# Kernel optimization log

Measured on AMD Instinct MI355X. Metric: run time of the kernel, lower is better.

The kernel has to match this reference:

```python
import jax, jax.numpy as jnp
import numpy as np

B, C, H, W = 2, 256, 128, 128
L, NH, NP = 4, 8, 4
D = C // NH
HW = H * W


def _pos_emb_2d(h, w, c):
    # positional_encodings.PositionalEncoding2D for channels-last input (B, h, w, c)
    ch = int(np.ceil(c / 4) * 2)
    inv_freq = 1.0 / (10000.0 ** (np.arange(0, ch, 2, dtype=np.float32) / ch))

    def emb(n):
        s = np.arange(n, dtype=np.float32)[:, None] * inv_freq[None, :]
        return np.stack([np.sin(s), np.cos(s)], -1).reshape(n, -1)  # interleaved sin/cos

    out = np.zeros((h, w, 2 * ch), np.float32)
    out[:, :, :ch] = emb(h)[:, None, :]
    out[:, :, ch:2 * ch] = emb(w)[None, :, :]
    return jnp.asarray(out[:, :, :c])


def _offset_bias():
    # init_weights grid_init bias of sampling_offsets
    thetas = np.arange(NH, dtype=np.float32) * (2.0 * np.pi / NH)
    g = np.stack([np.cos(thetas), np.sin(thetas)], -1)
    g = g / np.abs(g).max(-1, keepdims=True)
    g = np.tile(g[:, None, None, :], (1, 1, NP, 1))
    for i in range(NP):
        g[:, :, i, :] *= i + 1
    return np.tile(g.reshape(-1)[None], (L, 1)).astype(np.float32)


def _ref_points(h, w):
    # get_reference_points with scale_ratio == 1 (ratio of equal lidar ranges)
    ry, rx = jnp.meshgrid(jnp.linspace(0.5, h - 0.5, h) / h,
                          jnp.linspace(0.5, w - 0.5, w) / w, indexing='ij')
    return jnp.stack([rx.reshape(-1), ry.reshape(-1)], -1)  # (HW, 2) as (x, y)


def _deform_attn(value, loc, aw, h, w):
    # value: (B,HW,NH,D); loc in [0,1]: (B,HW,NH,NP,2); aw: (B,HW,NH,NP)
    # Matches F.grid_sample(mode='bilinear', padding_mode='zeros', align_corners=False)
    b, q, nh, d = value.shape
    p = loc.shape[3]
    v = value.transpose(0, 2, 1, 3)  # (B, NH, HW, D)
    gx = 2.0 * loc[..., 0] - 1.0
    gy = 2.0 * loc[..., 1] - 1.0
    ix = ((gx + 1.0) * w - 1.0) * 0.5
    iy = ((gy + 1.0) * h - 1.0) * 0.5
    x0 = jnp.floor(ix)
    y0 = jnp.floor(iy)

    def gather(xf, yf):
        valid = (xf >= 0) & (xf <= w - 1) & (yf >= 0) & (yf <= h - 1)
        xi = jnp.clip(xf, 0, w - 1).astype(jnp.int32)
        yi = jnp.clip(yf, 0, h - 1).astype(jnp.int32)
        idx = (yi * w + xi).transpose(0, 2, 1, 3).reshape(b, nh, q * p)
        g = jnp.take_along_axis(v, idx[..., None], axis=2).reshape(b, nh, q, p, d)
        return g * valid.transpose(0, 2, 1, 3)[..., None]

    wx1 = (ix - x0).transpose(0, 2, 1, 3)[..., None]
    wy1 = (iy - y0).transpose(0, 2, 1, 3)[..., None]
    wx0 = 1.0 - wx1
    wy0 = 1.0 - wy1
    s = (gather(x0, y0) * (wx0 * wy0) + gather(x0 + 1.0, y0) * (wx1 * wy0)
         + gather(x0, y0 + 1.0) * (wx0 * wy1) + gather(x0 + 1.0, y0 + 1.0) * (wx1 * wy1))
    out = jnp.einsum('bhqpd,bqhp->bqhd', s, aw)
    return out.reshape(b, q, nh * d)


def setup_inputs() -> dict:
    key = jax.random.key(0)
    ks = jax.random.split(key, 8)
    sc = 1.0 / np.sqrt(C).astype(np.float32)
    return {
        "ego_feature": jax.random.normal(ks[0], (B, C, H, W), jnp.float32),
        "conv_w": jax.random.normal(ks[1], (C, C), jnp.float32) * sc,  # 1x1 conv, (in,out)
        "conv_b": jnp.zeros((C,), jnp.float32),
        "in_scale": jnp.ones((1,), jnp.float32) / 30.0,
        "out_scale": jnp.ones((1,), jnp.float32) / 30.0,
        "off_w": jax.random.normal(ks[2], (L, C, NH * NP * 2), jnp.float32) * 0.01,
        "off_b": jnp.asarray(_offset_bias()),
        "aw_w": jax.random.normal(ks[3], (L, C, NH * NP), jnp.float32) * 0.02,
        "aw_b": jnp.zeros((L, NH * NP), jnp.float32),
        "vp_w": jax.random.normal(ks[4], (L, C, C), jnp.float32) * sc,
        "vp_b": jnp.zeros((L, C), jnp.float32),
        "op_w": jax.random.normal(ks[5], (L, C, C), jnp.float32) * sc,
        "op_b": jnp.zeros((L, C), jnp.float32),
    }


def reference(ego_feature, conv_w, conv_b, in_scale, out_scale, off_w, off_b,
              aw_w, aw_b, vp_w, vp_b, op_w, op_b):
    # PositionalEncodingPermute2D: channels-last PE, permuted to (C,H,W)
    pe_in = _pos_emb_2d(H, W, C).transpose(2, 0, 1)[None]  # (1,C,H,W)
    x = ego_feature + in_scale[0] * pe_in
    key_tok = x.reshape(B, C, HW).transpose(0, 2, 1)  # (B, HW, C)
    # Upsample(scale=1) is identity; 1x1 conv == per-token matmul
    out = key_tok @ conv_w + conv_b
    pe_out = _pos_emb_2d(H, W, C)[None]  # (1,H,W,C)
    ref = _ref_points(H, W)
    norm = jnp.asarray([W, H], jnp.float32)
    for l in range(L):
        o = out.reshape(B, H, W, C) + out_scale[0] * pe_out
        q = o.reshape(B, HW, C)
        identity = q
        v = (key_tok @ vp_w[l] + vp_b[l]).reshape(B, HW, NH, D)
        offs = (q @ off_w[l] + off_b[l]).reshape(B, HW, NH, NP, 2)
        aw = jax.nn.softmax((q @ aw_w[l] + aw_b[l]).reshape(B, HW, NH, NP), axis=-1)
        loc = ref[None, :, None, None, :] + offs / norm
        attn = _deform_attn(v, loc, aw, H, W)
        out = attn @ op_w[l] + op_b[l] + identity  # dropout is identity in eval
    return out  # (B, HW, C)
```

## Files before the change

kernel.cpp:

```cpp
#include <hip/hip_runtime.h>
#include <math.h>

#define HH 128
#define WW 128
#define CCH 256
#define NHH 8
#define NPP 4
#define DDIM 32
#define HWW (HH * WW)
#define BB 2
#define MM (BB * HWW)
#define KK 256

typedef __attribute__((ext_vector_type(8))) __bf16 bf16x8;
typedef __attribute__((ext_vector_type(8))) short s16x8;
typedef __attribute__((ext_vector_type(4))) short s16x4;
typedef __attribute__((ext_vector_type(4))) float f32x4;

#define PE_LOG2_STEP 0.20762050593f

__device__ __forceinline__ float pe_val(int c, int y, int x) {
    int j = (c & 127) >> 1;
    float pos = (c < 128) ? (float)y : (float)x;
    float f = exp2f(-(float)j * PE_LOG2_STEP);
    float s, cs;
    __sincosf(pos * f, &s, &cs);
    return (c & 1) ? cs : s;
}

__device__ __forceinline__ short f2b(float f) {
    union { float f; unsigned u; } c; c.f = f;
    unsigned r = c.u + 0x7FFF + ((c.u >> 16) & 1);
    return (short)(r >> 16);
}

__device__ __forceinline__ float b2f(short s) {
    union { unsigned u; float f; } c;
    c.u = ((unsigned)(unsigned short)s) << 16;
    return c.f;
}

__device__ __forceinline__ void gload16(const short* g, short* l) {
    __builtin_amdgcn_global_load_lds(
        (const __attribute__((address_space(1))) unsigned int*)g,
        (__attribute__((address_space(3))) unsigned int*)l, 16, 0, 0);
}

__global__ __launch_bounds__(256) void pe_table_kernel(
    const float* __restrict__ out_scale, short* __restrict__ pe_b)
{
    int t = blockIdx.x * 256 + threadIdx.x;
    int cp = t & 127;
    int p = t >> 7;
    int y = p >> 7, x = p & 127;
    int c2 = cp * 2;
    int j = (c2 & 127) >> 1;
    float pos = (c2 < 128) ? (float)y : (float)x;
    float f = exp2f(-(float)j * PE_LOG2_STEP);
    float s, c;
    __sincosf(pos * f, &s, &c);
    float sc = out_scale[0];
    pe_b[(size_t)p * CCH + c2] = f2b(sc * s);
    pe_b[(size_t)p * CCH + c2 + 1] = f2b(sc * c);
}

__global__ __launch_bounds__(256) void convert_big_w(
    const float* __restrict__ conv_w, const float* __restrict__ vp_w,
    const float* __restrict__ op_w, short* __restrict__ wt)
{
    __shared__ float tile[32][33];
    int z = blockIdx.z;
    const float* src = (z == 0) ? conv_w
                     : (z <= 4) ? vp_w + (size_t)(z - 1) * KK * CCH
                                : op_w + (size_t)(z - 5) * KK * CCH;
    short* dst = wt + (size_t)z * KK * CCH;
    int k0 = blockIdx.x * 32, n0 = blockIdx.y * 32;
    int tx = threadIdx.x, ty = threadIdx.y;
    #pragma unroll
    for (int i = 0; i < 4; ++i)
        tile[ty + i * 8][tx] = src[(size_t)(k0 + ty + i * 8) * CCH + n0 + tx];
    __syncthreads();
    int t = ty * 32 + tx;
    int n_l = t >> 3, ks = (t & 7) * 4;
    s16x4 o;
    #pragma unroll
    for (int j = 0; j < 4; ++j) o[j] = f2b(tile[ks + j][n_l]);
    *(s16x4*)&dst[(size_t)(n0 + n_l) * KK + k0 + ks] = o;
}

__global__ __launch_bounds__(256) void convert_offaw_w(
    const float* __restrict__ off_w, const float* __restrict__ aw_w,
    const float* __restrict__ off_b, const float* __restrict__ aw_b,
    short* __restrict__ wt, float* __restrict__ bias_cat)
{
    __shared__ float tile[32][33];
    int l = blockIdx.z;
    int nt = blockIdx.y;
    int k0 = blockIdx.x * 32;
    const float* src; int N, ncol0;
    if (nt < 2) { src = off_w + (size_t)l * KK * 64; N = 64; ncol0 = nt * 32; }
    else        { src = aw_w + (size_t)l * KK * 32; N = 32; ncol0 = 0; }
    int tx = threadIdx.x, ty = threadIdx.y;
    #pragma unroll
    for (int i = 0; i < 4; ++i)
        tile[ty + i * 8][tx] = src[(size_t)(k0 + ty + i * 8) * N + ncol0 + tx];
    __syncthreads();
    int t = ty * 32 + tx;
    int n_l = t >> 3, ks = (t & 7) * 4;
    s16x4 o;
    #pragma unroll
    for (int j = 0; j < 4; ++j) o[j] = f2b(tile[ks + j][n_l]);
    *(s16x4*)&wt[((size_t)l * 96 + nt * 32 + n_l) * KK + k0 + ks] = o;
    if (blockIdx.x == 0 && t < 32) {
        int col = nt * 32 + t;
        bias_cat[l * 96 + col] = (nt < 2) ? off_b[l * 64 + ncol0 + t]
                                          : aw_b[l * 32 + t];
    }
}

__global__ __launch_bounds__(256) void transpose_pe_kernel(
    const float* __restrict__ ego, const float* __restrict__ in_scale,
    short* __restrict__ ktb)
{
    __shared__ float tile[32][33];
    int b = blockIdx.z;
    int c0 = blockIdx.x * 32;
    int p0 = blockIdx.y * 32;
    int tx = threadIdx.x, ty = threadIdx.y;
    const float* egob = ego + (size_t)b * CCH * HWW;
    #pragma unroll
    for (int i = 0; i < 4; ++i)
        tile[ty + i * 8][tx] = egob[(size_t)(c0 + ty + i * 8) * HWW + p0 + tx];
    __syncthreads();
    float isc = in_scale[0];
    int t = ty * 32 + tx;
    int p_l = t >> 3, cs = (t & 7) * 4;
    int p = p0 + p_l;
    int y = p >> 7, x = p & 127;
    s16x4 o;
    #pragma unroll
    for (int j = 0; j < 4; ++j) {
        int c = c0 + cs + j;
        o[j] = f2b(tile[cs + j][p_l] + isc * pe_val(c, y, x));
    }
    *(s16x4*)&ktb[((size_t)b * HWW + p) * CCH + c0 + cs] = o;
}

template<int BN, int WM, int WN>
__device__ __forceinline__ void gemm_core_reg(
    const short* __restrict__ A, const short* __restrict__ Bt,
    short* As, short* Bs, int m0, int n0, int tid,
    f32x4 (&acc)[WM / 16][WN / 16])
{
    constexpr int MF = WM / 16, NF = WN / 16;
    constexpr int WAVES_N = BN / WN;
    constexpr int BTASK = BN / 32;
    int w = tid >> 6, lane = tid & 63;
    int g = lane >> 4, l16 = lane & 15;
    int wr = w / WAVES_N, wc = w % WAVES_N;

    s16x8 ra[4];
    s16x8 rb[BTASK];
    #pragma unroll
    for (int i = 0; i < 4; ++i) {
        int task = tid + i * 256; int r = task >> 3, s = task & 7;
        ra[i] = *(const s16x8*)(A + (size_t)(m0 + r) * KK + s * 8);
    }
    #pragma unroll
    for (int i = 0; i < BTASK; ++i) {
        int task = tid + i * 256; int r = task >> 3, s = task & 7;
        rb[i] = *(const s16x8*)(Bt + (size_t)(n0 + r) * KK + s * 8);
    }

    for (int ks = 0; ks < 4; ++ks) {
        __syncthreads();
        #pragma unroll
        for (int i = 0; i < 4; ++i) {
            int task = tid + i * 256; int r = task >> 3, s = task & 7;
            *(s16x8*)&As[r * 64 + ((s ^ (r & 7)) * 8)] = ra[i];
        }
        #pragma unroll
        for (int i = 0; i < BTASK; ++i) {
            int task = tid + i * 256; int r = task >> 3, s = task & 7;
            *(s16x8*)&Bs[r * 64 + ((s ^ (r & 7)) * 8)] = rb[i];
        }
        __syncthreads();
        if (ks < 3) {
            #pragma unroll
            for (int i = 0; i < 4; ++i) {
                int task = tid + i * 256; int r = task >> 3, s = task & 7;
                ra[i] = *(const s16x8*)(A + (size_t)(m0 + r) * KK + (ks + 1) * 64 + s * 8);
            }
            #pragma unroll
            for (int i = 0; i < BTASK; ++i) {
                int task = tid + i * 256; int r = task >> 3, s = task & 7;
                rb[i] = *(const s16x8*)(Bt + (size_t)(n0 + r) * KK + (ks + 1) * 64 + s * 8);
            }
        }
        #pragma unroll
        for (int kh = 0; kh < 2; ++kh) {
            bf16x8 af[MF], bfr[NF];
            #pragma unroll
            for (int mf = 0; mf < MF; ++mf) {
                int r = wr * WM + mf * 16 + l16, s = kh * 4 + g;
                af[mf] = *(const bf16x8*)(As + r * 64 + ((s ^ (r & 7)) * 8));
            }
            #pragma unroll
            for (int nf = 0; nf < NF; ++nf) {
                int r = wc * WN + nf * 16 + l16, s = kh * 4 + g;
                bfr[nf] = *(const bf16x8*)(Bs + r * 64 + ((s ^ (r & 7)) * 8));
            }
            #pragma unroll
            for (int mf = 0; mf < MF; ++mf)
                #pragma unroll
                for (int nf = 0; nf < NF; ++nf)
                    acc[mf][nf] = __builtin_amdgcn_mfma_f32_16x16x32_bf16(
                        af[mf], bfr[nf], acc[mf][nf], 0, 0, 0);
        }
    }
}

template<int NINST>
__device__ __forceinline__ void stage_tile(
    const short* __restrict__ src, short* dst, int row0, int ks, int w, int lane)
{
    #pragma unroll
    for (int i = 0; i < NINST; ++i) {
        int c = w * 64 + i * 256;
        int cc = c + lane;
        int r = cc >> 3, u = cc & 7;
        gload16(src + (size_t)(row0 + r) * KK + ks * 64 + ((u ^ (r & 7)) << 3),
                dst + c * 8);
    }
}

template<int BM, int BN, int WM, int WN>
__device__ __forceinline__ void gemm_core_db(
    const short* __restrict__ A, const short* __restrict__ Bt,
    short* AsBase, short* BsBase, int m0, int n0, int tid,
    f32x4 (&acc)[WM / 16][WN / 16])
{
    constexpr int MF = WM / 16, NF = WN / 16;
    constexpr int WAVES_N = BN / WN;
    constexpr int A_INST = (BM * 8) / 256;
    constexpr int B_INST = (BN * 8) / 256;
    int w = tid >> 6, lane = tid & 63;
    int g = lane >> 4, l16 = lane & 15;
    int wr = w / WAVES_N, wc = w % WAVES_N;
    short* As0 = AsBase; short* As1 = AsBase + BM * 64;
    short* Bs0 = BsBase; short* Bs1 = BsBase + BN * 64;

    stage_tile<A_INST>(A, As0, m0, 0, w, lane);
    stage_tile<B_INST>(Bt, Bs0, n0, 0, w, lane);
    asm volatile("s_waitcnt vmcnt(0)" ::: "memory");
    __syncthreads();

    #pragma unroll
    for (int ks = 0; ks < 4; ++ks) {
        short* Ac = (ks & 1) ? As1 : As0;
        short* Bc = (ks & 1) ? Bs1 : Bs0;
        short* An = (ks & 1) ? As0 : As1;
        short* Bn = (ks & 1) ? Bs0 : Bs1;
        if (ks < 3) {
            stage_tile<A_INST>(A, An, m0, ks + 1, w, lane);
            stage_tile<B_INST>(Bt, Bn, n0, ks + 1, w, lane);
        }
        #pragma unroll
        for (int kh = 0; kh < 2; ++kh) {
            bf16x8 af[MF], bfr[NF];
            #pragma unroll
            for (int mf = 0; mf < MF; ++mf) {
                int r = wr * WM + mf * 16 + l16, s = kh * 4 + g;
                af[mf] = *(const bf16x8*)(Ac + r * 64 + ((s ^ (r & 7)) * 8));
            }
            #pragma unroll
            for (int nf = 0; nf < NF; ++nf) {
                int r = wc * WN + nf * 16 + l16, s = kh * 4 + g;
                bfr[nf] = *(const bf16x8*)(Bc + r * 64 + ((s ^ (r & 7)) * 8));
            }
            #pragma unroll
            for (int mf = 0; mf < MF; ++mf)
                #pragma unroll
                for (int nf = 0; nf < NF; ++nf)
                    acc[mf][nf] = __builtin_amdgcn_mfma_f32_16x16x32_bf16(
                        af[mf], bfr[nf], acc[mf][nf], 0, 0, 0);
        }
        if (ks < 3) {
            __builtin_amdgcn_sched_barrier(0);
            asm volatile("s_waitcnt vmcnt(0)" ::: "memory");
            __syncthreads();
        }
    }
}

__global__ __launch_bounds__(256) void gemm_conv_v(
    const short* __restrict__ ktb, const short* __restrict__ wt_big,
    const float* __restrict__ conv_b, const float* __restrict__ vp_b,
    const short* __restrict__ pe_b, short* __restrict__ qb,
    short* __restrict__ vb16)
{
    __shared__ short As[128 * 64];
    __shared__ short Bs[128 * 64];
    int tid = threadIdx.x;
    int flat = blockIdx.x;
    int xcd = flat & 7;
    int idx = flat >> 3;
    int mloc = idx & 31;
    int rest = idx >> 5;
    int n0 = (rest & 1) * 128;
    int z = rest >> 1;
    int m0 = (xcd * 32 + mloc) * 128;

    f32x4 acc[4][4] = {};
    gemm_core_reg<128, 64, 64>(ktb, wt_big + (size_t)z * KK * CCH, As, Bs, m0, n0, tid, acc);

    int w = tid >> 6, lane = tid & 63;
    int g = lane >> 4, l16 = lane & 15;
    int wr = w >> 1, wc = w & 1;
    const float* bias = (z == 0) ? conv_b : vp_b + (size_t)(z - 1) * CCH;
    short* vz = vb16 + (size_t)(z - 1) * MM * CCH;
    #pragma unroll
    for (int mf = 0; mf < 4; ++mf) {
        #pragma unroll
        for (int nf = 0; nf < 4; ++nf) {
            int col = n0 + wc * 64 + nf * 16 + l16;
            float bv = bias[col];
            #pragma unroll
            for (int j = 0; j < 4; ++j) {
                int row = m0 + wr * 64 + mf * 16 + g * 4 + j;
                float vv = acc[mf][nf][j] + bv;
                if (z == 0) {
                    int p = row & (HWW - 1);
                    qb[(size_t)row * CCH + col] =
                        f2b(vv + b2f(pe_b[(size_t)p * CCH + col]));
                } else {
                    int b = row >> 14, p = row & (HWW - 1);
                    int h = col >> 5, d = col & 31;
                    vz[(((size_t)(b * NHH + h)) * HWW + p) * DDIM + d] = f2b(vv);
                }
            }
        }
    }
}

__global__ __launch_bounds__(256) void gemm_scores(
    const short* __restrict__ qb, const short* __restrict__ wt,
    const float* __restrict__ bias, float* __restrict__ scores)
{
    __shared__ short As[2 * 64 * 64];
    __shared__ short Bs[2 * 96 * 64];
    int tid = threadIdx.x;
    int m0 = blockIdx.y * 64;
    f32x4 acc[2][3] = {};
    gemm_core_db<64, 96, 32, 48>(qb, wt, As, Bs, m0, 0, tid, acc);

    int w = tid >> 6, lane = tid & 63;
    int g = lane >> 4, l16 = lane & 15;
    int wr = w >> 1, wc = w & 1;
    #pragma unroll
    for (int mf = 0; mf < 2; ++mf) {
        #pragma unroll
        for (int nf = 0; nf < 3; ++nf) {
            int col = wc * 48 + nf * 16 + l16;
            float bv = bias[col];
            #pragma unroll
            for (int j = 0; j < 4; ++j) {
                int row = m0 + wr * 32 + mf * 16 + g * 4 + j;
                scores[(size_t)row * 96 + col] = acc[mf][nf][j] + bv;
            }
        }
    }
}

template<bool FINAL>
__global__ __launch_bounds__(256) void gemm_op(
    const short* __restrict__ attnb, const short* __restrict__ wt,
    const float* __restrict__ bias, const short* __restrict__ pe_b,
    float* __restrict__ outf, short* __restrict__ qb)
{
    __shared__ short As[2 * 128 * 64];
    __shared__ short Bs[2 * 128 * 64];
    int tid = threadIdx.x;
    int flat = blockIdx.x;
    int xcd = flat & 7;
    int idx = flat >> 3;
    int mloc = idx & 31;
    int n0 = (idx >> 5) * 128;
    int m0 = (xcd * 32 + mloc) * 128;
    f32x4 acc[4][4] = {};
    gemm_core_db<128, 128, 64, 64>(attnb, wt, As, Bs, m0, n0, tid, acc);

    int w = tid >> 6, lane = tid & 63;
    int g = lane >> 4, l16 = lane & 15;
    int wr = w >> 1, wc = w & 1;
    #pragma unroll
    for (int mf = 0; mf < 4; ++mf) {
        #pragma unroll
        for (int nf = 0; nf < 4; ++nf) {
            int col = n0 + wc * 64 + nf * 16 + l16;
            float bv = bias[col];
            #pragma unroll
            for (int j = 0; j < 4; ++j) {
                int row = m0 + wr * 64 + mf * 16 + g * 4 + j;
                float vv = acc[mf][nf][j] + bv + b2f(qb[(size_t)row * CCH + col]);
                if (FINAL) {
                    outf[(size_t)row * CCH + col] = vv;
                } else {
                    int p = row & (HWW - 1);
                    qb[(size_t)row * CCH + col] =
                        f2b(vv + b2f(pe_b[(size_t)p * CCH + col]));
                }
            }
        }
    }
}

__device__ __forceinline__ void fma8(uint4 u, float w, float* a) {
    a[0] = fmaf(__uint_as_float(u.x << 16), w, a[0]);
    a[1] = fmaf(__uint_as_float(u.x & 0xffff0000u), w, a[1]);
    a[2] = fmaf(__uint_as_float(u.y << 16), w, a[2]);
    a[3] = fmaf(__uint_as_float(u.y & 0xffff0000u), w, a[3]);
    a[4] = fmaf(__uint_as_float(u.z << 16), w, a[4]);
    a[5] = fmaf(__uint_as_float(u.z & 0xffff0000u), w, a[5]);
    a[6] = fmaf(__uint_as_float(u.w << 16), w, a[6]);
    a[7] = fmaf(__uint_as_float(u.w & 0xffff0000u), w, a[7]);
}

__global__ __launch_bounds__(256) void deform_kernel(
    const short* __restrict__ vb16, const float* __restrict__ scores,
    short* __restrict__ attnb)
{
    int tid = threadIdx.x;
    int gi = tid >> 2;
    int dl = (tid & 3) * 8;
    long gid = (long)blockIdx.x * 64 + gi;
    int h = (int)(gid & 7);
    long bp = gid >> 3;
    int p = (int)(bp & (HWW - 1));
    int b = (int)(bp >> 14);
    int y = p >> 7, x = p & 127;
    const float* srow = scores + bp * 96;
    float4 sc4 = *(const float4*)(srow + 64 + h * 4);
    float mx = fmaxf(fmaxf(sc4.x, sc4.y), fmaxf(sc4.z, sc4.w));
    float e0 = __expf(sc4.x - mx), e1 = __expf(sc4.y - mx);
    float e2 = __expf(sc4.z - mx), e3 = __expf(sc4.w - mx);
    float inv = 1.f / (e0 + e1 + e2 + e3);
    float wa4[4] = {e0 * inv, e1 * inv, e2 * inv, e3 * inv};
    float4 o01 = *(const float4*)(srow + h * 8);
    float4 o23 = *(const float4*)(srow + h * 8 + 4);
    float oxs[4] = {o01.x, o01.z, o23.x, o23.z};
    float oys[4] = {o01.y, o01.w, o23.y, o23.w};
    const short* vbase = vb16 + ((size_t)(b * NHH + h) * HWW) * DDIM + dl;
    float a[8] = {};
    #pragma unroll
    for (int pt = 0; pt < NPP; ++pt) {
        float wa = wa4[pt];
        float ix = (float)x + oxs[pt];
        float iy = (float)y + oys[pt];
        float x0f = floorf(ix), y0f = floorf(iy);
        float fx = ix - x0f, fy = iy - y0f;
        float wx0 = (x0f >= 0.f && x0f <= 127.f) ? (1.f - fx) : 0.f;
        float wx1 = (x0f >= -1.f && x0f <= 126.f) ? fx : 0.f;
        float wy0 = ((y0f >= 0.f && y0f <= 127.f) ? (1.f - fy) : 0.f) * wa;
        float wy1 = ((y0f >= -1.f && y0f <= 126.f) ? fy : 0.f) * wa;
        int xi0 = (int)fminf(fmaxf(x0f, 0.f), 127.f);
        int yi0 = (int)fminf(fmaxf(y0f, 0.f), 127.f);
        int xi1 = (int)fminf(fmaxf(x0f + 1.f, 0.f), 127.f);
        int yi1 = (int)fminf(fmaxf(y0f + 1.f, 0.f), 127.f);
        int r0 = yi0 << 7, r1 = yi1 << 7;
        uint4 u00 = *(const uint4*)(vbase + (size_t)(r0 + xi0) * DDIM);
        uint4 u01 = *(const uint4*)(vbase + (size_t)(r0 + xi1) * DDIM);
        uint4 u10 = *(const uint4*)(vbase + (size_t)(r1 + xi0) * DDIM);
        uint4 u11 = *(const uint4*)(vbase + (size_t)(r1 + xi1) * DDIM);
        fma8(u00, wx0 * wy0, a);
        fma8(u01, wx1 * wy0, a);
        fma8(u10, wx0 * wy1, a);
        fma8(u11, wx1 * wy1, a);
    }
    s16x8 o;
    #pragma unroll
    for (int j = 0; j < 8; ++j) o[j] = f2b(a[j]);
    *(s16x8*)&attnb[bp * CCH + h * DDIM + dl] = o;
}

extern "C" void kernel_launch(void* const* d_in, const int* in_sizes, int n_in,
                              void* d_out, int out_size, void* d_ws, size_t ws_size,
                              hipStream_t stream) {
    const float* ego       = (const float*)d_in[0];
    const float* conv_w    = (const float*)d_in[1];
    const float* conv_b    = (const float*)d_in[2];
    const float* in_scale  = (const float*)d_in[3];
    const float* out_scale = (const float*)d_in[4];
    const float* off_w     = (const float*)d_in[5];
    const float* off_b     = (const float*)d_in[6];
    const float* aw_w      = (const float*)d_in[7];
    const float* aw_b      = (const float*)d_in[8];
    const float* vp_w      = (const float*)d_in[9];
    const float* vp_b      = (const float*)d_in[10];
    const float* op_w      = (const float*)d_in[11];
    const float* op_b      = (const float*)d_in[12];
    float* out = (float*)d_out;

    float* scores   = (float*)d_ws;
    float* bias_cat = scores + (size_t)MM * 96;
    short* pe_b     = (short*)(bias_cat + 4 * 96);
    short* ktb      = pe_b + (size_t)HWW * CCH;
    short* qb       = ktb + (size_t)MM * CCH;
    short* vb16     = qb + (size_t)MM * CCH;
    short* attnb    = vb16 + (size_t)4 * MM * CCH;
    short* wt_big   = attnb + (size_t)MM * CCH;
    short* wt_offaw = wt_big + (size_t)9 * KK * CCH;

    pe_table_kernel<<<HWW * 128 / 256, 256, 0, stream>>>(out_scale, pe_b);
    convert_big_w<<<dim3(8, 8, 9), dim3(32, 8), 0, stream>>>(conv_w, vp_w, op_w, wt_big);
    convert_offaw_w<<<dim3(8, 3, 4), dim3(32, 8), 0, stream>>>(
        off_w, aw_w, off_b, aw_b, wt_offaw, bias_cat);
    transpose_pe_kernel<<<dim3(8, 512, 2), dim3(32, 8), 0, stream>>>(ego, in_scale, ktb);

    gemm_conv_v<<<2560, 256, 0, stream>>>(
        ktb, wt_big, conv_b, vp_b, pe_b, qb, vb16);

    for (int l = 0; l < 4; ++l) {
        gemm_scores<<<dim3(1, 512), 256, 0, stream>>>(
            qb, wt_offaw + (size_t)l * 96 * KK, bias_cat + l * 96, scores);
        deform_kernel<<<MM * NHH / 64, 256, 0, stream>>>(
            vb16 + (size_t)l * MM * CCH, scores, attnb);
        if (l < 3) {
            gemm_op<false><<<512, 256, 0, stream>>>(
                attnb, wt_big + (size_t)(5 + l) * KK * CCH, op_b + l * CCH,
                pe_b, nullptr, qb);
        } else {
            gemm_op<true><<<512, 256, 0, stream>>>(
                attnb, wt_big + (size_t)(5 + l) * KK * CCH, op_b + l * CCH,
                pe_b, out, qb);
        }
    }
}
```

Measured before the change: 226.9 us.

## Keep A slab resident in LDS and loop over all five weight matrices

The conv+value-projection GEMM now loads a 64x256 A slab once into shared memory and iterates over all five weight matrices (conv plus four value projections) inside one block, instead of launching a separate block per weight matrix that reloads A. B tiles are prefetched through registers across k-steps and across z. This cuts redundant global reads of the activation matrix at the cost of fewer blocks (1024 vs 2560), a larger LDS footprint, and serialized work per block.

```diff
diff --git a/kernel.cpp b/kernel.cpp
--- a/kernel.cpp
+++ b/kernel.cpp
@@ -146,6 +146,19 @@
     *(s16x4*)&ktb[((size_t)b * HWW + p) * CCH + c0 + cs] = o;
 }
 
+__device__ __forceinline__ void stage_slab64(
+    const short* __restrict__ src, short* As, int m0, int w, int lane)
+{
+    #pragma unroll
+    for (int i = 0; i < 8; ++i) {
+        int c = w * 64 + i * 256;
+        int cc = c + lane;
+        int r = cc >> 5, col = cc & 31, ks = col >> 3, u = col & 7;
+        gload16(src + (size_t)(m0 + r) * KK + ks * 64 + ((u ^ (r & 7)) << 3),
+                As + c * 8);
+    }
+}
+
 template<int BN, int WM, int WN>
 __device__ __forceinline__ void gemm_core_reg(
     const short* __restrict__ A, const short* __restrict__ Bt,
@@ -299,44 +312,97 @@
     const short* __restrict__ pe_b, short* __restrict__ qb,
     short* __restrict__ vb16)
 {
-    __shared__ short As[128 * 64];
+    __shared__ short As[64 * 256];
     __shared__ short Bs[128 * 64];
     int tid = threadIdx.x;
+    int w = tid >> 6, lane = tid & 63;
+    int g = lane >> 4, l16 = lane & 15;
+    int wr = w >> 1, wc = w & 1;
     int flat = blockIdx.x;
     int xcd = flat & 7;
     int idx = flat >> 3;
-    int mloc = idx & 31;
-    int rest = idx >> 5;
-    int n0 = (rest & 1) * 128;
-    int z = rest >> 1;
-    int m0 = (xcd * 32 + mloc) * 128;
-
-    f32x4 acc[4][4] = {};
-    gemm_core_reg<128, 64, 64>(ktb, wt_big + (size_t)z * KK * CCH, As, Bs, m0, n0, tid, acc);
-
-    int w = tid >> 6, lane = tid & 63;
-    int g = lane >> 4, l16 = lane & 15;
-    int wr = w >> 1, wc = w & 1;
-    const float* bias = (z == 0) ? conv_b : vp_b + (size_t)(z - 1) * CCH;
-    short* vz = vb16 + (size_t)(z - 1) * MM * CCH;
-    #pragma unroll
-    for (int mf = 0; mf < 4; ++mf) {
+    int mloc = idx & 63;
+    int n0 = (idx >> 6) * 128;
+    int m0 = (xcd * 64 + mloc) * 64;
+
+    stage_slab64(ktb, As, m0, w, lane);
+    s16x8 rb[4];
+    #pragma unroll
+    for (int i = 0; i < 4; ++i) {
+        int task = tid + i * 256; int r = task >> 3, s = task & 7;
+        rb[i] = *(const s16x8*)(wt_big + (size_t)(n0 + r) * KK + s * 8);
+    }
+    asm volatile("s_waitcnt vmcnt(0)" ::: "memory");
+    __syncthreads();
+
+    for (int z = 0; z < 5; ++z) {
+        f32x4 acc[2][4] = {};
+        for (int ks = 0; ks < 4; ++ks) {
+            __syncthreads();
+            #pragma unroll
+            for (int i = 0; i < 4; ++i) {
+                int task = tid + i * 256; int r = task >> 3, s = task & 7;
+                *(s16x8*)&Bs[r * 64 + ((s ^ (r & 7)) * 8)] = rb[i];
+            }
+            __syncthreads();
+            if (ks < 3) {
+                const short* Bz = wt_big + (size_t)z * KK * CCH;
+                #pragma unroll
+                for (int i = 0; i < 4; ++i) {
+                    int task = tid + i * 256; int r = task >> 3, s = task & 7;
+                    rb[i] = *(const s16x8*)(Bz + (size_t)(n0 + r) * KK + (ks + 1) * 64 + s * 8);
+                }
+            } else if (z < 4) {
+                const short* Bz = wt_big + (size_t)(z + 1) * KK * CCH;
+                #pragma unroll
+                for (int i = 0; i < 4; ++i) {
+                    int task = tid + i * 256; int r = task >> 3, s = task & 7;
+                    rb[i] = *(const s16x8*)(Bz + (size_t)(n0 + r) * KK + s * 8);
+                }
+            }
+            #pragma unroll
+            for (int kh = 0; kh < 2; ++kh) {
+                int s = kh * 4 + g;
+                bf16x8 af[2], bfr[4];
+                #pragma unroll
+                for (int mf = 0; mf < 2; ++mf) {
+                    int r = wr * 32 + mf * 16 + l16;
+                    af[mf] = *(const bf16x8*)(As + r * 256 + (ks * 8 + (s ^ (r & 7))) * 8);
+                }
+                #pragma unroll
+                for (int nf = 0; nf < 4; ++nf) {
+                    int r = wc * 64 + nf * 16 + l16;
+                    bfr[nf] = *(const bf16x8*)(Bs + r * 64 + ((s ^ (r & 7)) * 8));
+                }
+                #pragma unroll
+                for (int mf = 0; mf < 2; ++mf)
+                    #pragma unroll
+                    for (int nf = 0; nf < 4; ++nf)
+                        acc[mf][nf] = __builtin_amdgcn_mfma_f32_16x16x32_bf16(
+                            af[mf], bfr[nf], acc[mf][nf], 0, 0, 0);
+            }
+        }
+        const float* bias = (z == 0) ? conv_b : vp_b + (size_t)(z - 1) * CCH;
+        short* vz = vb16 + (size_t)(z - 1) * MM * CCH;
         #pragma unroll
-        for (int nf = 0; nf < 4; ++nf) {
-            int col = n0 + wc * 64 + nf * 16 + l16;
-            float bv = bias[col];
-            #pragma unroll
-            for (int j = 0; j < 4; ++j) {
-                int row = m0 + wr * 64 + mf * 16 + g * 4 + j;
-                float vv = acc[mf][nf][j] + bv;
-                if (z == 0) {
-                    int p = row & (HWW - 1);
-                    qb[(size_t)row * CCH + col] =
-                        f2b(vv + b2f(pe_b[(size_t)p * CCH + col]));
-                } else {
-                    int b = row >> 14, p = row & (HWW - 1);
-                    int h = col >> 5, d = col & 31;
-                    vz[(((size_t)(b * NHH + h)) * HWW + p) * DDIM + d] = f2b(vv);
+        for (int mf = 0; mf < 2; ++mf) {
+            #pragma unroll
+            for (int nf = 0; nf < 4; ++nf) {
+                int col = n0 + wc * 64 + nf * 16 + l16;
+                float bv = bias[col];
+                #pragma unroll
+                for (int j = 0; j < 4; ++j) {
+                    int row = m0 + wr * 32 + mf * 16 + g * 4 + j;
+                    float vv = acc[mf][nf][j] + bv;
+                    if (z == 0) {
+                        int p = row & (HWW - 1);
+                        qb[(size_t)row * CCH + col] =
+                            f2b(vv + b2f(pe_b[(size_t)p * CCH + col]));
+                    } else {
+                        int b = row >> 14, p = row & (HWW - 1);
+                        int h = col >> 5, d = col & 31;
+                        vz[(((size_t)(b * NHH + h)) * HWW + p) * DDIM + d] = f2b(vv);
+                    }
                 }
             }
         }
@@ -517,7 +583,7 @@
         off_w, aw_w, off_b, aw_b, wt_offaw, bias_cat);
     transpose_pe_kernel<<<dim3(8, 512, 2), dim3(32, 8), 0, stream>>>(ego, in_scale, ktb);
 
-    gemm_conv_v<<<2560, 256, 0, stream>>>(
+    gemm_conv_v<<<1024, 256, 0, stream>>>(
         ktb, wt_big, conv_b, vp_b, pe_b, qb, vb16);
 
     for (int l = 0; l < 4; ++l) {
```

New measurement: 214.3 us. 5.5% less time.

## Keep A slab resident across five weight GEMMs and tile deform kernel spatially per head

Applied to the files above, without the earlier changes.

The conv+value-projection GEMM now loads a 64-row slab of key tokens (full K=256) into shared memory once and loops over all five weight matrices, double-buffering the B tiles in registers and LDS. This cuts the repeated A reads that came from launching separate blocks per z. The deform kernel is remapped so each block handles an 8x8 spatial tile of one (batch, head), with (batch, head) pairs spread across XCDs, to improve locality of the bilinear gathers in L2. The trade-offs are fewer, longer GEMM blocks with more shared memory (lower occupancy and a serial z loop), and strided score reads in the deform kernel.

```diff
diff --git a/kernel.cpp b/kernel.cpp
--- a/kernel.cpp
+++ b/kernel.cpp
@@ -146,77 +146,16 @@
     *(s16x4*)&ktb[((size_t)b * HWW + p) * CCH + c0 + cs] = o;
 }
 
-template<int BN, int WM, int WN>
-__device__ __forceinline__ void gemm_core_reg(
-    const short* __restrict__ A, const short* __restrict__ Bt,
-    short* As, short* Bs, int m0, int n0, int tid,
-    f32x4 (&acc)[WM / 16][WN / 16])
-{
-    constexpr int MF = WM / 16, NF = WN / 16;
-    constexpr int WAVES_N = BN / WN;
-    constexpr int BTASK = BN / 32;
-    int w = tid >> 6, lane = tid & 63;
-    int g = lane >> 4, l16 = lane & 15;
-    int wr = w / WAVES_N, wc = w % WAVES_N;
-
-    s16x8 ra[4];
-    s16x8 rb[BTASK];
-    #pragma unroll
-    for (int i = 0; i < 4; ++i) {
-        int task = tid + i * 256; int r = task >> 3, s = task & 7;
-        ra[i] = *(const s16x8*)(A + (size_t)(m0 + r) * KK + s * 8);
-    }
-    #pragma unroll
-    for (int i = 0; i < BTASK; ++i) {
-        int task = tid + i * 256; int r = task >> 3, s = task & 7;
-        rb[i] = *(const s16x8*)(Bt + (size_t)(n0 + r) * KK + s * 8);
-    }
-
-    for (int ks = 0; ks < 4; ++ks) {
-        __syncthreads();
-        #pragma unroll
-        for (int i = 0; i < 4; ++i) {
-            int task = tid + i * 256; int r = task >> 3, s = task & 7;
-            *(s16x8*)&As[r * 64 + ((s ^ (r & 7)) * 8)] = ra[i];
-        }
-        #pragma unroll
-        for (int i = 0; i < BTASK; ++i) {
-            int task = tid + i * 256; int r = task >> 3, s = task & 7;
-            *(s16x8*)&Bs[r * 64 + ((s ^ (r & 7)) * 8)] = rb[i];
-        }
-        __syncthreads();
-        if (ks < 3) {
-            #pragma unroll
-            for (int i = 0; i < 4; ++i) {
-                int task = tid + i * 256; int r = task >> 3, s = task & 7;
-                ra[i] = *(const s16x8*)(A + (size_t)(m0 + r) * KK + (ks + 1) * 64 + s * 8);
-            }
-            #pragma unroll
-            for (int i = 0; i < BTASK; ++i) {
-                int task = tid + i * 256; int r = task >> 3, s = task & 7;
-                rb[i] = *(const s16x8*)(Bt + (size_t)(n0 + r) * KK + (ks + 1) * 64 + s * 8);
-            }
-        }
-        #pragma unroll
-        for (int kh = 0; kh < 2; ++kh) {
-            bf16x8 af[MF], bfr[NF];
-            #pragma unroll
-            for (int mf = 0; mf < MF; ++mf) {
-                int r = wr * WM + mf * 16 + l16, s = kh * 4 + g;
-                af[mf] = *(const bf16x8*)(As + r * 64 + ((s ^ (r & 7)) * 8));
-            }
-            #pragma unroll
-            for (int nf = 0; nf < NF; ++nf) {
-                int r = wc * WN + nf * 16 + l16, s = kh * 4 + g;
-                bfr[nf] = *(const bf16x8*)(Bs + r * 64 + ((s ^ (r & 7)) * 8));
-            }
-            #pragma unroll
-            for (int mf = 0; mf < MF; ++mf)
-                #pragma unroll
-                for (int nf = 0; nf < NF; ++nf)
-                    acc[mf][nf] = __builtin_amdgcn_mfma_f32_16x16x32_bf16(
-                        af[mf], bfr[nf], acc[mf][nf], 0, 0, 0);
-        }
+__device__ __forceinline__ void stage_slab64(
+    const short* __restrict__ src, short* As, int m0, int w, int lane)
+{
+    #pragma unroll
+    for (int i = 0; i < 8; ++i) {
+        int c = w * 64 + i * 256;
+        int cc = c + lane;
+        int r = cc >> 5, col = cc & 31, ks = col >> 3, u = col & 7;
+        gload16(src + (size_t)(m0 + r) * KK + ks * 64 + ((u ^ (r & 7)) << 3),
+                As + c * 8);
     }
 }
 
@@ -299,44 +238,92 @@
     const short* __restrict__ pe_b, short* __restrict__ qb,
     short* __restrict__ vb16)
 {
-    __shared__ short As[128 * 64];
-    __shared__ short Bs[128 * 64];
+    __shared__ short As[64 * 256];
+    __shared__ short Bs[2 * 128 * 64];
     int tid = threadIdx.x;
+    int w = tid >> 6, lane = tid & 63;
+    int g = lane >> 4, l16 = lane & 15;
+    int wr = w >> 1, wc = w & 1;
     int flat = blockIdx.x;
     int xcd = flat & 7;
     int idx = flat >> 3;
-    int mloc = idx & 31;
-    int rest = idx >> 5;
-    int n0 = (rest & 1) * 128;
-    int z = rest >> 1;
-    int m0 = (xcd * 32 + mloc) * 128;
-
-    f32x4 acc[4][4] = {};
-    gemm_core_reg<128, 64, 64>(ktb, wt_big + (size_t)z * KK * CCH, As, Bs, m0, n0, tid, acc);
-
-    int w = tid >> 6, lane = tid & 63;
-    int g = lane >> 4, l16 = lane & 15;
-    int wr = w >> 1, wc = w & 1;
-    const float* bias = (z == 0) ? conv_b : vp_b + (size_t)(z - 1) * CCH;
-    short* vz = vb16 + (size_t)(z - 1) * MM * CCH;
-    #pragma unroll
-    for (int mf = 0; mf < 4; ++mf) {
+    int mloc = idx & 63;
+    int n0 = (idx >> 6) * 128;
+    int m0 = (xcd * 64 + mloc) * 64;
+
+    stage_slab64(ktb, As, m0, w, lane);
+    s16x8 rb[4];
+    #pragma unroll
+    for (int i = 0; i < 4; ++i) {
+        int task = tid + i * 256; int r = task >> 3, s = task & 7;
+        rb[i] = *(const s16x8*)(wt_big + (size_t)(n0 + r) * KK + s * 8);
+    }
+    asm volatile("s_waitcnt vmcnt(0)" ::: "memory");
+    __syncthreads();
+
+    for (int z = 0; z < 5; ++z) {
+        f32x4 acc[2][4] = {};
+        for (int ks = 0; ks < 4; ++ks) {
+            int t = z * 4 + ks;
+            short* Bcur = Bs + (t & 1) * (128 * 64);
+            #pragma unroll
+            for (int i = 0; i < 4; ++i) {
+                int task = tid + i * 256; int r = task >> 3, s = task & 7;
+                *(s16x8*)&Bcur[r * 64 + ((s ^ (r & 7)) * 8)] = rb[i];
+            }
+            __syncthreads();
+            if (t < 19) {
+                int tn = t + 1;
+                const short* Bz = wt_big + (size_t)(tn >> 2) * KK * CCH + (tn & 3) * 64;
+                #pragma unroll
+                for (int i = 0; i < 4; ++i) {
+                    int task = tid + i * 256; int r = task >> 3, s = task & 7;
+                    rb[i] = *(const s16x8*)(Bz + (size_t)(n0 + r) * KK + s * 8);
+                }
+            }
+            #pragma unroll
+            for (int kh = 0; kh < 2; ++kh) {
+                int s = kh * 4 + g;
+                bf16x8 af[2], bfr[4];
+                #pragma unroll
+                for (int mf = 0; mf < 2; ++mf) {
+                    int r = wr * 32 + mf * 16 + l16;
+                    af[mf] = *(const bf16x8*)(As + r * 256 + (ks * 8 + (s ^ (r & 7))) * 8);
+                }
+                #pragma unroll
+                for (int nf = 0; nf < 4; ++nf) {
+                    int r = wc * 64 + nf * 16 + l16;
+                    bfr[nf] = *(const bf16x8*)(Bcur + r * 64 + ((s ^ (r & 7)) * 8));
+                }
+                #pragma unroll
+                for (int mf = 0; mf < 2; ++mf)
+                    #pragma unroll
+                    for (int nf = 0; nf < 4; ++nf)
+                        acc[mf][nf] = __builtin_amdgcn_mfma_f32_16x16x32_bf16(
+                            af[mf], bfr[nf], acc[mf][nf], 0, 0, 0);
+            }
+        }
+        const float* bias = (z == 0) ? conv_b : vp_b + (size_t)(z - 1) * CCH;
+        short* vz = vb16 + (size_t)(z - 1) * MM * CCH;
         #pragma unroll
-        for (int nf = 0; nf < 4; ++nf) {
-            int col = n0 + wc * 64 + nf * 16 + l16;
-            float bv = bias[col];
-            #pragma unroll
-            for (int j = 0; j < 4; ++j) {
-                int row = m0 + wr * 64 + mf * 16 + g * 4 + j;
-                float vv = acc[mf][nf][j] + bv;
-                if (z == 0) {
-                    int p = row & (HWW - 1);
-                    qb[(size_t)row * CCH + col] =
-                        f2b(vv + b2f(pe_b[(size_t)p * CCH + col]));
-                } else {
-                    int b = row >> 14, p = row & (HWW - 1);
-                    int h = col >> 5, d = col & 31;
-                    vz[(((size_t)(b * NHH + h)) * HWW + p) * DDIM + d] = f2b(vv);
+        for (int mf = 0; mf < 2; ++mf) {
+            #pragma unroll
+            for (int nf = 0; nf < 4; ++nf) {
+                int col = n0 + wc * 64 + nf * 16 + l16;
+                float bv = bias[col];
+                #pragma unroll
+                for (int j = 0; j < 4; ++j) {
+                    int row = m0 + wr * 32 + mf * 16 + g * 4 + j;
+                    float vv = acc[mf][nf][j] + bv;
+                    if (z == 0) {
+                        int p = row & (HWW - 1);
+                        qb[(size_t)row * CCH + col] =
+                            f2b(vv + b2f(pe_b[(size_t)p * CCH + col]));
+                    } else {
+                        int b = row >> 14, p = row & (HWW - 1);
+                        int h = col >> 5, d = col & 31;
+                        vz[(((size_t)(b * NHH + h)) * HWW + p) * DDIM + d] = f2b(vv);
+                    }
                 }
             }
         }
@@ -433,12 +420,16 @@
     int tid = threadIdx.x;
     int gi = tid >> 2;
     int dl = (tid & 3) * 8;
-    long gid = (long)blockIdx.x * 64 + gi;
-    int h = (int)(gid & 7);
-    long bp = gid >> 3;
-    int p = (int)(bp & (HWW - 1));
-    int b = (int)(bp >> 14);
-    int y = p >> 7, x = p & 127;
+    int flat = blockIdx.x;
+    int xcd = flat & 7;
+    int idx = flat >> 3;
+    int bh = xcd * 2 + (idx >> 8);
+    int tile = idx & 255;
+    int b = bh >> 3, h = bh & 7;
+    int y = (tile >> 4) * 8 + (gi >> 3);
+    int x = (tile & 15) * 8 + (gi & 7);
+    int p = (y << 7) + x;
+    long bp = (long)b * HWW + p;
     const float* srow = scores + bp * 96;
     float4 sc4 = *(const float4*)(srow + 64 + h * 4);
     float mx = fmaxf(fmaxf(sc4.x, sc4.y), fmaxf(sc4.z, sc4.w));
@@ -450,7 +441,7 @@
     float4 o23 = *(const float4*)(srow + h * 8 + 4);
     float oxs[4] = {o01.x, o01.z, o23.x, o23.z};
     float oys[4] = {o01.y, o01.w, o23.y, o23.w};
-    const short* vbase = vb16 + ((size_t)(b * NHH + h) * HWW) * DDIM + dl;
+    const short* vbase = vb16 + ((size_t)bh * HWW) * DDIM + dl;
     float a[8] = {};
     #pragma unroll
     for (int pt = 0; pt < NPP; ++pt) {
@@ -517,13 +508,13 @@
         off_w, aw_w, off_b, aw_b, wt_offaw, bias_cat);
     transpose_pe_kernel<<<dim3(8, 512, 2), dim3(32, 8), 0, stream>>>(ego, in_scale, ktb);
 
-    gemm_conv_v<<<2560, 256, 0, stream>>>(
+    gemm_conv_v<<<1024, 256, 0, stream>>>(
         ktb, wt_big, conv_b, vp_b, pe_b, qb, vb16);
 
     for (int l = 0; l < 4; ++l) {
         gemm_scores<<<dim3(1, 512), 256, 0, stream>>>(
             qb, wt_offaw + (size_t)l * 96 * KK, bias_cat + l * 96, scores);
-        deform_kernel<<<MM * NHH / 64, 256, 0, stream>>>(
+        deform_kernel<<<4096, 256, 0, stream>>>(
             vb16 + (size_t)l * MM * CCH, scores, attnb);
         if (l < 3) {
             gemm_op<false><<<512, 256, 0, stream>>>(
```

Measured after the change: 224.6 us. About the same (-1.0%).
